# Optimization experiments

Measured on AMD Instinct MI355X. Metric: run time of the kernel, lower is better.

## Reference

```python
import jax, jax.numpy as jnp
import numpy as np

N = 50000      # nodes
E = 800000     # edges (before self-loops)
IN = 128       # in_channels
HID = 32       # hidden_channels
HEADS = 4
OUT = 2        # out_channels
NEG_SLOPE = 0.2  # PyG GATConv default LeakyReLU slope


def gat_layer(x, src, dst, W, a_src, a_dst, b, n_nodes, concat):
    """PyG GATConv (eval mode, self-loops already appended to src/dst).
    x: [N, in], W: [in, H*F], a_src/a_dst: [H, F], b: [H*F] or [F].
    """
    H, F = a_src.shape
    h = (x @ W).reshape(n_nodes, H, F)              # [N, H, F]
    al_s = (h * a_src).sum(-1)                      # [N, H] per-node src logit
    al_d = (h * a_dst).sum(-1)                      # [N, H] per-node dst logit
    e = al_s[src] + al_d[dst]                       # [E', H]
    e = jnp.where(e > 0, e, NEG_SLOPE * e)          # LeakyReLU
    # segment softmax over edges grouped by destination node
    m = jax.ops.segment_max(e, dst, num_segments=n_nodes)
    m = jnp.where(jnp.isfinite(m), m, 0.0)
    num = jnp.exp(e - m[dst])                       # [E', H]
    den = jax.ops.segment_sum(num, dst, num_segments=n_nodes)
    alpha = num / (den[dst] + 1e-16)                # [E', H]
    out = jax.ops.segment_sum(alpha[:, :, None] * h[src], dst, num_segments=n_nodes)  # [N, H, F]
    out = out.reshape(n_nodes, H * F) if concat else out.mean(axis=1)
    return out + b


def setup_inputs() -> dict:
    key = jax.random.key(0)
    ks = jax.random.split(key, 16)
    HID4 = HID // 4
    inp = {
        "x": jax.random.normal(ks[0], (N, IN), dtype=jnp.float32),
        "edge_index": jax.random.randint(ks[1], (2, E), 0, N, dtype=jnp.int64),
        "edge_attr": jax.random.normal(ks[2], (E, 8), dtype=jnp.float32),
        # conv1: in=IN -> HID per head, HEADS heads, concat
        "W1": jax.random.normal(ks[3], (IN, HEADS * HID), dtype=jnp.float32) * (1.0 / np.sqrt(IN)),
        "a_src1": jax.random.normal(ks[4], (HEADS, HID), dtype=jnp.float32) * 0.1,
        "a_dst1": jax.random.normal(ks[5], (HEADS, HID), dtype=jnp.float32) * 0.1,
        "b1": jnp.zeros((HEADS * HID,), dtype=jnp.float32),
        # conv2: in=HEADS*HID -> HID//4, 1 head, mean (concat=False)
        "W2": jax.random.normal(ks[6], (HEADS * HID, HID4), dtype=jnp.float32) * (1.0 / np.sqrt(HEADS * HID)),
        "a_src2": jax.random.normal(ks[7], (1, HID4), dtype=jnp.float32) * 0.1,
        "a_dst2": jax.random.normal(ks[8], (1, HID4), dtype=jnp.float32) * 0.1,
        "b2": jnp.zeros((HID4,), dtype=jnp.float32),
        # final linear
        "Wl": jax.random.normal(ks[9], (HID4, OUT), dtype=jnp.float32) * (1.0 / np.sqrt(HID4)),
        "bl": jnp.zeros((OUT,), dtype=jnp.float32),
    }
    return inp


def reference(x, edge_index, edge_attr, W1, a_src1, a_dst1, b1,
              W2, a_src2, a_dst2, b2, Wl, bl):
    # edge_attr is ignored (GATConv built without edge_dim). Eval mode: dropout is identity.
    loop = jnp.arange(N, dtype=edge_index.dtype)
    src = jnp.concatenate([edge_index[0], loop])  # PyG adds self-loops by default
    dst = jnp.concatenate([edge_index[1], loop])
    h = jax.nn.elu(gat_layer(x, src, dst, W1, a_src1, a_dst1, b1, N, concat=True))
    h = jax.nn.elu(gat_layer(h, src, dst, W2, a_src2, a_dst2, b2, N, concat=False))
    return jax.nn.sigmoid(h @ Wl + bl)
```

## Files before the change

### kernel.cpp

```cpp
#include <hip/hip_runtime.h>
#include <math.h>

#define TPB 256
#define BN 64
#define BK 32
#define CAP 64
#define LOG2E 1.44269504088896f

__device__ __forceinline__ float elu_f(float x)  { return x > 0.f ? x : __expf(x) - 1.f; }
__device__ __forceinline__ float sigmoid_f(float x){ return 1.f / (1.f + __expf(-x)); }
__device__ __forceinline__ float leaky(float x)  { return fmaxf(x, 0.2f * x); }

__device__ __forceinline__ unsigned int f2bf(float f) {
    unsigned int u = __float_as_uint(f);
    return (u + 0x7FFFu + ((u >> 16) & 1u)) >> 16;
}
__device__ __forceinline__ float bf_lo(unsigned int u) { return __uint_as_float(u << 16); }
__device__ __forceinline__ float bf_hi(unsigned int u) { return __uint_as_float(u & 0xffff0000u); }

static inline int cdiv(long long a, int b) { return (int)((a + b - 1) / b); }

__global__ __launch_bounds__(256) void gemm1_tiled(
        const float* __restrict__ x, const float* __restrict__ W,
        const float* __restrict__ a_src, const float* __restrict__ a_dst,
        unsigned short* __restrict__ hb, float* __restrict__ als, float* __restrict__ ald,
        int* __restrict__ cursor, int N) {
    if (threadIdx.x < BN) {
        int i = blockIdx.x * BN + threadIdx.x;
        if (i < N) cursor[i] = 0;
    }
    __shared__ float xs[BN][BK + 1];
    __shared__ float wsh[BK][128];
    int tid = threadIdx.x;
    int tx = tid & 15, ty = tid >> 4;
    int n0 = blockIdx.x * BN;

    float acc[4][8];
#pragma unroll
    for (int r = 0; r < 4; r++)
#pragma unroll
        for (int c = 0; c < 8; c++) acc[r][c] = 0.f;

    for (int k0 = 0; k0 < 128; k0 += BK) {
#pragma unroll
        for (int i = 0; i < 2; i++) {
            int r = (tid >> 3) + i * 32;
            int kk = (tid & 7) * 4;
            int row = n0 + r;
            float4 v = (row < N) ? *(const float4*)(x + (size_t)row * 128 + k0 + kk)
                                 : make_float4(0.f, 0.f, 0.f, 0.f);
            *(float4*)(&xs[r][kk]) = v;
        }
#pragma unroll
        for (int i = 0; i < 4; i++) {
            int idx = tid + i * 256;
            int kr = idx >> 5, c4 = (idx & 31) * 4;
            *(float4*)(&wsh[kr][c4]) = *(const float4*)(W + (size_t)(k0 + kr) * 128 + c4);
        }
        __syncthreads();
#pragma unroll
        for (int k = 0; k < BK; k++) {
            float a[4], bf[8];
#pragma unroll
            for (int i = 0; i < 4; i++) a[i] = xs[ty * 4 + i][k];
            float4 b0 = *(const float4*)(&wsh[k][tx * 8]);
            float4 b1 = *(const float4*)(&wsh[k][tx * 8 + 4]);
            bf[0] = b0.x; bf[1] = b0.y; bf[2] = b0.z; bf[3] = b0.w;
            bf[4] = b1.x; bf[5] = b1.y; bf[6] = b1.z; bf[7] = b1.w;
#pragma unroll
            for (int r = 0; r < 4; r++)
#pragma unroll
                for (int c = 0; c < 8; c++)
                    acc[r][c] = fmaf(a[r], bf[c], acc[r][c]);
        }
        __syncthreads();
    }

    float asr[8], adr[8];
#pragma unroll
    for (int i = 0; i < 8; i++) {
        asr[i] = a_src[tx * 8 + i];
        adr[i] = a_dst[tx * 8 + i];
    }
    int hd = tx >> 2;
#pragma unroll
    for (int r = 0; r < 4; r++) {
        int row = n0 + ty * 4 + r;
        float ps = 0.f, pd = 0.f;
#pragma unroll
        for (int i = 0; i < 8; i++) {
            ps = fmaf(acc[r][i], asr[i], ps);
            pd = fmaf(acc[r][i], adr[i], pd);
        }
        ps += __shfl_xor(ps, 1); ps += __shfl_xor(ps, 2);
        pd += __shfl_xor(pd, 1); pd += __shfl_xor(pd, 2);
        if (row < N) {
            uint4 o;
            o.x = f2bf(acc[r][0]) | (f2bf(acc[r][1]) << 16);
            o.y = f2bf(acc[r][2]) | (f2bf(acc[r][3]) << 16);
            o.z = f2bf(acc[r][4]) | (f2bf(acc[r][5]) << 16);
            o.w = f2bf(acc[r][6]) | (f2bf(acc[r][7]) << 16);
            *(uint4*)(hb + (size_t)row * 128 + tx * 8) = o;
            if ((tx & 3) == 0) {
                als[row * 4 + hd] = ps * LOG2E;
                ald[row * 4 + hd] = pd * LOG2E;
            }
        }
    }
}

__global__ void scatter_kernel(const int* __restrict__ ei, int E, int N, int gsz,
                               int* __restrict__ cursor, unsigned short* __restrict__ slots) {
    int myg = blockIdx.x & 7;
    int e = (blockIdx.x >> 3) * blockDim.x + threadIdx.x;
    if (e >= E + N) return;
    int d = (e < E) ? ei[E + e] : (e - E);
    if (d / gsz != myg) return;
    int s = (e < E) ? ei[e] : d;
    int pos = atomicAdd(&cursor[d], 1);
    if (pos < CAP) slots[((size_t)d << 6) + pos] = (unsigned short)s;
}

__global__ void accum1_fused(const int* __restrict__ cursor, const unsigned short* __restrict__ slots,
                             const unsigned short* __restrict__ hb,
                             const float* __restrict__ als, const float* __restrict__ ald,
                             const float* __restrict__ b, const float* __restrict__ W2,
                             const float* __restrict__ a_src2, const float* __restrict__ a_dst2,
                             float* __restrict__ h2, float* __restrict__ als2,
                             float* __restrict__ ald2, int N) {
    int t = blockIdx.x * blockDim.x + threadIdx.x;
    int n = t >> 6;
    if (n >= N) return;
    int lane = t & 63;
    int eslot = lane >> 4;
    int fg = lane & 15;
    int hd = fg >> 2;

    float ald_h = ald[n * 4 + hd];
    int cnt = cursor[n];
    const unsigned short* cp = slots + ((size_t)n << 6);

    int i0 = eslot < cnt ? eslot : cnt - 1;
    int s_c = cp[i0];
    float al_c = als[s_c * 4 + hd];
    uint4 u_c = *(const uint4*)(hb + (size_t)s_c * 128 + fg * 8);

    float acc[8];
#pragma unroll
    for (int k = 0; k < 8; k++) acc[k] = 0.f;
    float den = 0.f;

    for (int base = 0; base < cnt; base += 4) {
        int nxt = base + 4 + eslot;
        int ic = nxt < cnt ? nxt : cnt - 1;
        int s_n = cp[ic];
        float al_n = als[s_n * 4 + hd];
        uint4 u_n = *(const uint4*)(hb + (size_t)s_n * 128 + fg * 8);

        float w = exp2f(leaky(al_c + ald_h));
        if (base + eslot >= cnt) w = 0.f;
        acc[0] = fmaf(w, bf_lo(u_c.x), acc[0]);
        acc[1] = fmaf(w, bf_hi(u_c.x), acc[1]);
        acc[2] = fmaf(w, bf_lo(u_c.y), acc[2]);
        acc[3] = fmaf(w, bf_hi(u_c.y), acc[3]);
        acc[4] = fmaf(w, bf_lo(u_c.z), acc[4]);
        acc[5] = fmaf(w, bf_hi(u_c.z), acc[5]);
        acc[6] = fmaf(w, bf_lo(u_c.w), acc[6]);
        acc[7] = fmaf(w, bf_hi(u_c.w), acc[7]);
        den += w;

        al_c = al_n; u_c = u_n;
    }

#pragma unroll
    for (int k = 0; k < 8; k++) {
        acc[k] += __shfl_xor(acc[k], 16);
        acc[k] += __shfl_xor(acc[k], 32);
    }
    den += __shfl_xor(den, 16);
    den += __shfl_xor(den, 32);

    float inv = 1.f / (den + 1e-16f);
    float bv[8];
    *(float4*)(bv)     = *(const float4*)(b + fg * 8);
    *(float4*)(bv + 4) = *(const float4*)(b + fg * 8 + 4);
    float o[8];
#pragma unroll
    for (int k = 0; k < 8; k++) o[k] = elu_f(acc[k] * inv + bv[k]);

    int srcl = lane >> 2;
    float tmp[8];
#pragma unroll
    for (int k = 0; k < 8; k++) tmp[k] = __shfl(o[k], srcl);
    int sel = lane & 3;
    float o0 = sel == 0 ? tmp[0] : sel == 1 ? tmp[2] : sel == 2 ? tmp[4] : tmp[6];
    float o1 = sel == 0 ? tmp[1] : sel == 1 ? tmp[3] : sel == 2 ? tmp[5] : tmp[7];

    float w2a[8], w2b[8];
#pragma unroll
    for (int c = 0; c < 8; c += 4) {
        *(float4*)(w2a + c) = *(const float4*)(W2 + (size_t)(2 * lane) * 8 + c);
        *(float4*)(w2b + c) = *(const float4*)(W2 + (size_t)(2 * lane + 1) * 8 + c);
    }
    float part[8];
#pragma unroll
    for (int c = 0; c < 8; c++)
        part[c] = fmaf(o0, w2a[c], o1 * w2b[c]);
#pragma unroll
    for (int c = 0; c < 8; c++) {
        part[c] += __shfl_xor(part[c], 1);
        part[c] += __shfl_xor(part[c], 2);
        part[c] += __shfl_xor(part[c], 4);
    }
    int ch = lane & 7;
    float v = part[0];
    v = ch == 1 ? part[1] : v;  v = ch == 2 ? part[2] : v;  v = ch == 3 ? part[3] : v;
    v = ch == 4 ? part[4] : v;  v = ch == 5 ? part[5] : v;  v = ch == 6 ? part[6] : v;
    v = ch == 7 ? part[7] : v;
    v += __shfl_xor(v, 8); v += __shfl_xor(v, 16); v += __shfl_xor(v, 32);
    if (lane < 8) h2[(size_t)n * 8 + lane] = v;
    float ps = v * a_src2[ch];
    float pd = v * a_dst2[ch];
    ps += __shfl_xor(ps, 1); ps += __shfl_xor(ps, 2); ps += __shfl_xor(ps, 4);
    pd += __shfl_xor(pd, 1); pd += __shfl_xor(pd, 2); pd += __shfl_xor(pd, 4);
    if (lane == 0) {
        als2[n] = ps * LOG2E;
        ald2[n] = pd * LOG2E;
    }
}

__global__ void accum2_final(const int* __restrict__ cursor, const unsigned short* __restrict__ slots,
                             const float* __restrict__ h2,
                             const float* __restrict__ als, const float* __restrict__ ald,
                             const float* __restrict__ b2, const float* __restrict__ Wl,
                             const float* __restrict__ bl, float* __restrict__ out, int N) {
    int t = blockIdx.x * blockDim.x + threadIdx.x;
    int n = t >> 6;
    if (n >= N) return;
    int lane = t & 63;
    int slot = lane >> 3;
    int c = lane & 7;

    float ald_n = ald[n];
    int cnt = cursor[n];
    const unsigned short* cp = slots + ((size_t)n << 6);

    int i0 = slot < cnt ? slot : cnt - 1;
    int s_c = cp[i0];
    float al_c = als[s_c];
    float h_c = h2[(size_t)s_c * 8 + c];

    float den = 0.f, acc = 0.f;
    for (int base = 0; base < cnt; base += 8) {
        int nxt = base + 8 + slot;
        int ic = nxt < cnt ? nxt : cnt - 1;
        int s_n = cp[ic];
        float al_n = als[s_n];
        float h_n = h2[(size_t)s_n * 8 + c];

        float w = exp2f(leaky(al_c + ald_n));
        if (base + slot >= cnt) w = 0.f;
        acc = fmaf(w, h_c, acc);
        den += w;

        al_c = al_n; h_c = h_n;
    }
    acc += __shfl_xor(acc, 8);  acc += __shfl_xor(acc, 16); acc += __shfl_xor(acc, 32);
    den += __shfl_xor(den, 8);  den += __shfl_xor(den, 16); den += __shfl_xor(den, 32);

    float inv = 1.f / (den + 1e-16f);
    float o = elu_f(acc * inv + b2[c]);
    float r0 = o * Wl[c * 2 + 0];
    float r1 = o * Wl[c * 2 + 1];
    r0 += __shfl_xor(r0, 1); r0 += __shfl_xor(r0, 2); r0 += __shfl_xor(r0, 4);
    r1 += __shfl_xor(r1, 1); r1 += __shfl_xor(r1, 2); r1 += __shfl_xor(r1, 4);
    if (lane == 0) {
        float2 r;
        r.x = sigmoid_f(r0 + bl[0]);
        r.y = sigmoid_f(r1 + bl[1]);
        *(float2*)(out + (size_t)n * 2) = r;
    }
}

extern "C" void kernel_launch(void* const* d_in, const int* in_sizes, int n_in,
                              void* d_out, int out_size, void* d_ws, size_t ws_size,
                              hipStream_t stream) {
    const float* x      = (const float*)d_in[0];
    const int*   ei     = (const int*)d_in[1];
    const float* W1     = (const float*)d_in[3];
    const float* a_src1 = (const float*)d_in[4];
    const float* a_dst1 = (const float*)d_in[5];
    const float* b1     = (const float*)d_in[6];
    const float* W2     = (const float*)d_in[7];
    const float* a_src2 = (const float*)d_in[8];
    const float* a_dst2 = (const float*)d_in[9];
    const float* b2     = (const float*)d_in[10];
    const float* Wl     = (const float*)d_in[11];
    const float* bl     = (const float*)d_in[12];
    float* out = (float*)d_out;

    const int N = in_sizes[0] / 128;
    const int E = in_sizes[1] / 2;
    const int EN = E + N;
    const int gsz = cdiv(N, 8);

    unsigned short* h1b = (unsigned short*)d_ws;
    float* als1 = (float*)d_ws + (size_t)N * 64;
    float* ald1 = als1 + (size_t)N * 4;
    float* h2   = ald1 + (size_t)N * 4;
    float* als2 = h2   + (size_t)N * 8;
    float* ald2 = als2 + (size_t)N;
    int* cursor = (int*)(ald2 + (size_t)N);
    unsigned short* slots = (unsigned short*)(cursor + N);
    (void)ws_size; (void)n_in; (void)out_size;

    gemm1_tiled<<<cdiv(N, BN), 256, 0, stream>>>(x, W1, a_src1, a_dst1, h1b, als1, ald1, cursor, N);
    scatter_kernel<<<8 * cdiv(EN, TPB), TPB, 0, stream>>>(ei, E, N, gsz, cursor, slots);
    accum1_fused<<<cdiv((long long)N * 64, TPB), TPB, 0, stream>>>(
        cursor, slots, h1b, als1, ald1, b1, W2, a_src2, a_dst2, h2, als2, ald2, N);
    accum2_final<<<cdiv((long long)N * 64, TPB), TPB, 0, stream>>>(
        cursor, slots, h2, als2, ald2, b2, Wl, bl, out, N);
}
```

Baseline: 236.2 us.

## Use bf16 MFMA for first GEMM, handle self-loops inline, two edges per scatter thread

Replaces the FP32 tiled GEMM with a bf16 MFMA 16x16x32 kernel. x and a transposed W are staged as bf16 in shared memory, and the attention logits are reduced with shuffles. Self-loops are no longer scattered into slots; the accumulation kernels add the self-term directly, so each node's slot list and the atomic traffic shrink. The scatter kernel now handles two edges per thread and replaces the integer group divide with a float multiply. Rounding the GEMM inputs to bf16 lowers precision, and the float-based group test could misassign nodes at group boundaries.

After: 235.7 us. No clear change (-0.2%).

```diff
diff --git a/kernel.cpp b/kernel.cpp
--- a/kernel.cpp
+++ b/kernel.cpp
@@ -2,123 +2,148 @@
 #include <math.h>
 
 #define TPB 256
-#define BN 64
-#define BK 32
+#define GN 64
 #define CAP 64
 #define LOG2E 1.44269504088896f
+
+typedef short bf16x8 __attribute__((ext_vector_type(8)));
+typedef float floatx4 __attribute__((ext_vector_type(4)));
 
 __device__ __forceinline__ float elu_f(float x)  { return x > 0.f ? x : __expf(x) - 1.f; }
 __device__ __forceinline__ float sigmoid_f(float x){ return 1.f / (1.f + __expf(-x)); }
 __device__ __forceinline__ float leaky(float x)  { return fmaxf(x, 0.2f * x); }
 
-__device__ __forceinline__ unsigned int f2bf(float f) {
+__device__ __forceinline__ unsigned short f2bf(float f) {
     unsigned int u = __float_as_uint(f);
-    return (u + 0x7FFFu + ((u >> 16) & 1u)) >> 16;
+    return (unsigned short)((u + 0x7FFFu + ((u >> 16) & 1u)) >> 16);
 }
 __device__ __forceinline__ float bf_lo(unsigned int u) { return __uint_as_float(u << 16); }
 __device__ __forceinline__ float bf_hi(unsigned int u) { return __uint_as_float(u & 0xffff0000u); }
 
 static inline int cdiv(long long a, int b) { return (int)((a + b - 1) / b); }
 
-__global__ __launch_bounds__(256) void gemm1_tiled(
+__global__ __launch_bounds__(256) void gemm1_mfma(
         const float* __restrict__ x, const float* __restrict__ W,
         const float* __restrict__ a_src, const float* __restrict__ a_dst,
         unsigned short* __restrict__ hb, float* __restrict__ als, float* __restrict__ ald,
         int* __restrict__ cursor, int N) {
-    if (threadIdx.x < BN) {
-        int i = blockIdx.x * BN + threadIdx.x;
-        if (i < N) cursor[i] = 0;
-    }
-    __shared__ float xs[BN][BK + 1];
-    __shared__ float wsh[BK][128];
+    __shared__ unsigned short xs[GN][136];
+    __shared__ unsigned short wt[128][136];
     int tid = threadIdx.x;
-    int tx = tid & 15, ty = tid >> 4;
-    int n0 = blockIdx.x * BN;
-
-    float acc[4][8];
-#pragma unroll
-    for (int r = 0; r < 4; r++)
-#pragma unroll
-        for (int c = 0; c < 8; c++) acc[r][c] = 0.f;
-
-    for (int k0 = 0; k0 < 128; k0 += BK) {
-#pragma unroll
-        for (int i = 0; i < 2; i++) {
-            int r = (tid >> 3) + i * 32;
-            int kk = (tid & 7) * 4;
-            int row = n0 + r;
-            float4 v = (row < N) ? *(const float4*)(x + (size_t)row * 128 + k0 + kk)
-                                 : make_float4(0.f, 0.f, 0.f, 0.f);
-            *(float4*)(&xs[r][kk]) = v;
-        }
-#pragma unroll
-        for (int i = 0; i < 4; i++) {
-            int idx = tid + i * 256;
-            int kr = idx >> 5, c4 = (idx & 31) * 4;
-            *(float4*)(&wsh[kr][c4]) = *(const float4*)(W + (size_t)(k0 + kr) * 128 + c4);
-        }
-        __syncthreads();
-#pragma unroll
-        for (int k = 0; k < BK; k++) {
-            float a[4], bf[8];
-#pragma unroll
-            for (int i = 0; i < 4; i++) a[i] = xs[ty * 4 + i][k];
-            float4 b0 = *(const float4*)(&wsh[k][tx * 8]);
-            float4 b1 = *(const float4*)(&wsh[k][tx * 8 + 4]);
-            bf[0] = b0.x; bf[1] = b0.y; bf[2] = b0.z; bf[3] = b0.w;
-            bf[4] = b1.x; bf[5] = b1.y; bf[6] = b1.z; bf[7] = b1.w;
-#pragma unroll
-            for (int r = 0; r < 4; r++)
-#pragma unroll
-                for (int c = 0; c < 8; c++)
-                    acc[r][c] = fmaf(a[r], bf[c], acc[r][c]);
-        }
-        __syncthreads();
+    int n0 = blockIdx.x * GN;
+    if (tid < GN) { int i = n0 + tid; if (i < N) cursor[i] = 0; }
+
+#pragma unroll
+    for (int i = 0; i < 8; i++) {
+        int idx = tid + i * 256;
+        int r = idx >> 5;
+        int c4 = (idx & 31) * 4;
+        int row = n0 + r; if (row >= N) row = N - 1;
+        float4 v = *(const float4*)(x + (size_t)row * 128 + c4);
+        unsigned short* p = &xs[r][c4];
+        p[0] = f2bf(v.x); p[1] = f2bf(v.y); p[2] = f2bf(v.z); p[3] = f2bf(v.w);
+    }
+#pragma unroll
+    for (int i = 0; i < 16; i++) {
+        int idx = tid + i * 256;
+        int k = idx >> 5;
+        int c4 = (idx & 31) * 4;
+        float4 v = *(const float4*)(W + (size_t)k * 128 + c4);
+        wt[c4 + 0][k] = f2bf(v.x);
+        wt[c4 + 1][k] = f2bf(v.y);
+        wt[c4 + 2][k] = f2bf(v.z);
+        wt[c4 + 3][k] = f2bf(v.w);
+    }
+    __syncthreads();
+
+    int w = tid >> 6;
+    int lane = tid & 63;
+    int idx16 = lane & 15, quad = lane >> 4;
+    int nw = n0 + w * 16;
+
+    bf16x8 af[4];
+#pragma unroll
+    for (int kc = 0; kc < 4; kc++)
+        af[kc] = *(const bf16x8*)(&xs[w * 16 + idx16][kc * 32 + quad * 8]);
+
+    floatx4 accs[8];
+#pragma unroll
+    for (int cg = 0; cg < 8; cg++) {
+        floatx4 acc = {0.f, 0.f, 0.f, 0.f};
+#pragma unroll
+        for (int kc = 0; kc < 4; kc++) {
+            bf16x8 bf = *(const bf16x8*)(&wt[cg * 16 + idx16][kc * 32 + quad * 8]);
+            acc = __builtin_amdgcn_mfma_f32_16x16x32_bf16(af[kc], bf, acc, 0, 0, 0);
+        }
+        accs[cg] = acc;
     }
 
     float asr[8], adr[8];
 #pragma unroll
-    for (int i = 0; i < 8; i++) {
-        asr[i] = a_src[tx * 8 + i];
-        adr[i] = a_dst[tx * 8 + i];
-    }
-    int hd = tx >> 2;
-#pragma unroll
-    for (int r = 0; r < 4; r++) {
-        int row = n0 + ty * 4 + r;
-        float ps = 0.f, pd = 0.f;
-#pragma unroll
-        for (int i = 0; i < 8; i++) {
-            ps = fmaf(acc[r][i], asr[i], ps);
-            pd = fmaf(acc[r][i], adr[i], pd);
-        }
-        ps += __shfl_xor(ps, 1); ps += __shfl_xor(ps, 2);
-        pd += __shfl_xor(pd, 1); pd += __shfl_xor(pd, 2);
-        if (row < N) {
-            uint4 o;
-            o.x = f2bf(acc[r][0]) | (f2bf(acc[r][1]) << 16);
-            o.y = f2bf(acc[r][2]) | (f2bf(acc[r][3]) << 16);
-            o.z = f2bf(acc[r][4]) | (f2bf(acc[r][5]) << 16);
-            o.w = f2bf(acc[r][6]) | (f2bf(acc[r][7]) << 16);
-            *(uint4*)(hb + (size_t)row * 128 + tx * 8) = o;
-            if ((tx & 3) == 0) {
-                als[row * 4 + hd] = ps * LOG2E;
-                ald[row * 4 + hd] = pd * LOG2E;
-            }
-        }
-    }
-}
-
-__global__ void scatter_kernel(const int* __restrict__ ei, int E, int N, int gsz,
+    for (int cg = 0; cg < 8; cg++) {
+        asr[cg] = a_src[cg * 16 + idx16];
+        adr[cg] = a_dst[cg * 16 + idx16];
+    }
+    float ps[16], pd[16];
+#pragma unroll
+    for (int i = 0; i < 16; i++) { ps[i] = 0.f; pd[i] = 0.f; }
+#pragma unroll
+    for (int cg = 0; cg < 8; cg++) {
+        int h = cg >> 1;
+#pragma unroll
+        for (int r = 0; r < 4; r++) {
+            ps[r * 4 + h] = fmaf(accs[cg][r], asr[cg], ps[r * 4 + h]);
+            pd[r * 4 + h] = fmaf(accs[cg][r], adr[cg], pd[r * 4 + h]);
+        }
+    }
+#pragma unroll
+    for (int i = 0; i < 16; i++) {
+        ps[i] += __shfl_xor(ps[i], 1); ps[i] += __shfl_xor(ps[i], 2);
+        ps[i] += __shfl_xor(ps[i], 4); ps[i] += __shfl_xor(ps[i], 8);
+        pd[i] += __shfl_xor(pd[i], 1); pd[i] += __shfl_xor(pd[i], 2);
+        pd[i] += __shfl_xor(pd[i], 4); pd[i] += __shfl_xor(pd[i], 8);
+    }
+    float myps = 0.f, mypd = 0.f;
+#pragma unroll
+    for (int i = 0; i < 16; i++) {
+        if (i == idx16) { myps = ps[i]; mypd = pd[i]; }
+    }
+    int rowl = nw + quad * 4 + (idx16 >> 2);
+    if (rowl < N) {
+        als[rowl * 4 + (idx16 & 3)] = myps * LOG2E;
+        ald[rowl * 4 + (idx16 & 3)] = mypd * LOG2E;
+    }
+#pragma unroll
+    for (int cg = 0; cg < 8; cg++) {
+#pragma unroll
+        for (int r = 0; r < 4; r++) {
+            int row = nw + quad * 4 + r;
+            if (row < N) hb[(size_t)row * 128 + cg * 16 + idx16] = f2bf(accs[cg][r]);
+        }
+    }
+}
+
+__global__ void scatter_kernel(const int* __restrict__ ei, int E, float invg,
                                int* __restrict__ cursor, unsigned short* __restrict__ slots) {
     int myg = blockIdx.x & 7;
-    int e = (blockIdx.x >> 3) * blockDim.x + threadIdx.x;
-    if (e >= E + N) return;
-    int d = (e < E) ? ei[E + e] : (e - E);
-    if (d / gsz != myg) return;
-    int s = (e < E) ? ei[e] : d;
-    int pos = atomicAdd(&cursor[d], 1);
-    if (pos < CAP) slots[((size_t)d << 6) + pos] = (unsigned short)s;
+    int p = (blockIdx.x >> 3) * blockDim.x + threadIdx.x;
+    int e0 = p * 2;
+    if (e0 >= E) return;
+    int d0 = ei[E + e0];
+    if ((int)((float)d0 * invg) == myg) {
+        int s = ei[e0];
+        int pos = atomicAdd(&cursor[d0], 1);
+        if (pos < CAP) slots[((size_t)d0 << 6) + pos] = (unsigned short)s;
+    }
+    int e1 = e0 + 1;
+    if (e1 < E) {
+        int d1 = ei[E + e1];
+        if ((int)((float)d1 * invg) == myg) {
+            int s = ei[e1];
+            int pos = atomicAdd(&cursor[d1], 1);
+            if (pos < CAP) slots[((size_t)d1 << 6) + pos] = (unsigned short)s;
+        }
+    }
 }
 
 __global__ void accum1_fused(const int* __restrict__ cursor, const unsigned short* __restrict__ slots,
@@ -140,36 +165,46 @@
     int cnt = cursor[n];
     const unsigned short* cp = slots + ((size_t)n << 6);
 
-    int i0 = eslot < cnt ? eslot : cnt - 1;
-    int s_c = cp[i0];
-    float al_c = als[s_c * 4 + hd];
-    uint4 u_c = *(const uint4*)(hb + (size_t)s_c * 128 + fg * 8);
-
     float acc[8];
 #pragma unroll
     for (int k = 0; k < 8; k++) acc[k] = 0.f;
     float den = 0.f;
-
-    for (int base = 0; base < cnt; base += 4) {
-        int nxt = base + 4 + eslot;
-        int ic = nxt < cnt ? nxt : cnt - 1;
-        int s_n = cp[ic];
-        float al_n = als[s_n * 4 + hd];
-        uint4 u_n = *(const uint4*)(hb + (size_t)s_n * 128 + fg * 8);
-
-        float w = exp2f(leaky(al_c + ald_h));
-        if (base + eslot >= cnt) w = 0.f;
-        acc[0] = fmaf(w, bf_lo(u_c.x), acc[0]);
-        acc[1] = fmaf(w, bf_hi(u_c.x), acc[1]);
-        acc[2] = fmaf(w, bf_lo(u_c.y), acc[2]);
-        acc[3] = fmaf(w, bf_hi(u_c.y), acc[3]);
-        acc[4] = fmaf(w, bf_lo(u_c.z), acc[4]);
-        acc[5] = fmaf(w, bf_hi(u_c.z), acc[5]);
-        acc[6] = fmaf(w, bf_lo(u_c.w), acc[6]);
-        acc[7] = fmaf(w, bf_hi(u_c.w), acc[7]);
-        den += w;
-
-        al_c = al_n; u_c = u_n;
+    if (eslot == 0) {
+        float wself = exp2f(leaky(als[n * 4 + hd] + ald_h));
+        uint4 us = *(const uint4*)(hb + (size_t)n * 128 + fg * 8);
+        acc[0] = wself * bf_lo(us.x); acc[1] = wself * bf_hi(us.x);
+        acc[2] = wself * bf_lo(us.y); acc[3] = wself * bf_hi(us.y);
+        acc[4] = wself * bf_lo(us.z); acc[5] = wself * bf_hi(us.z);
+        acc[6] = wself * bf_lo(us.w); acc[7] = wself * bf_hi(us.w);
+        den = wself;
+    }
+
+    if (cnt > 0) {
+        int i0 = eslot < cnt ? eslot : cnt - 1;
+        int s_c = cp[i0];
+        float al_c = als[s_c * 4 + hd];
+        uint4 u_c = *(const uint4*)(hb + (size_t)s_c * 128 + fg * 8);
+        for (int base = 0; base < cnt; base += 4) {
+            int nxt = base + 4 + eslot;
+            int ic = nxt < cnt ? nxt : cnt - 1;
+            int s_n = cp[ic];
+            float al_n = als[s_n * 4 + hd];
+            uint4 u_n = *(const uint4*)(hb + (size_t)s_n * 128 + fg * 8);
+
+            float w = exp2f(leaky(al_c + ald_h));
+            if (base + eslot >= cnt) w = 0.f;
+            acc[0] = fmaf(w, bf_lo(u_c.x), acc[0]);
+            acc[1] = fmaf(w, bf_hi(u_c.x), acc[1]);
+            acc[2] = fmaf(w, bf_lo(u_c.y), acc[2]);
+            acc[3] = fmaf(w, bf_hi(u_c.y), acc[3]);
+            acc[4] = fmaf(w, bf_lo(u_c.z), acc[4]);
+            acc[5] = fmaf(w, bf_hi(u_c.z), acc[5]);
+            acc[6] = fmaf(w, bf_lo(u_c.w), acc[6]);
+            acc[7] = fmaf(w, bf_hi(u_c.w), acc[7]);
+            den += w;
+
+            al_c = al_n; u_c = u_n;
+        }
     }
 
 #pragma unroll
@@ -245,25 +280,32 @@
     int cnt = cursor[n];
     const unsigned short* cp = slots + ((size_t)n << 6);
 
-    int i0 = slot < cnt ? slot : cnt - 1;
-    int s_c = cp[i0];
-    float al_c = als[s_c];
-    float h_c = h2[(size_t)s_c * 8 + c];
-
     float den = 0.f, acc = 0.f;
-    for (int base = 0; base < cnt; base += 8) {
-        int nxt = base + 8 + slot;
-        int ic = nxt < cnt ? nxt : cnt - 1;
-        int s_n = cp[ic];
-        float al_n = als[s_n];
-        float h_n = h2[(size_t)s_n * 8 + c];
-
-        float w = exp2f(leaky(al_c + ald_n));
-        if (base + slot >= cnt) w = 0.f;
-        acc = fmaf(w, h_c, acc);
-        den += w;
-
-        al_c = al_n; h_c = h_n;
+    if (slot == 0) {
+        float wself = exp2f(leaky(als[n] + ald_n));
+        acc = wself * h2[(size_t)n * 8 + c];
+        den = wself;
+    }
+
+    if (cnt > 0) {
+        int i0 = slot < cnt ? slot : cnt - 1;
+        int s_c = cp[i0];
+        float al_c = als[s_c];
+        float h_c = h2[(size_t)s_c * 8 + c];
+        for (int base = 0; base < cnt; base += 8) {
+            int nxt = base + 8 + slot;
+            int ic = nxt < cnt ? nxt : cnt - 1;
+            int s_n = cp[ic];
+            float al_n = als[s_n];
+            float h_n = h2[(size_t)s_n * 8 + c];
+
+            float w = exp2f(leaky(al_c + ald_n));
+            if (base + slot >= cnt) w = 0.f;
+            acc = fmaf(w, h_c, acc);
+            den += w;
+
+            al_c = al_n; h_c = h_n;
+        }
     }
     acc += __shfl_xor(acc, 8);  acc += __shfl_xor(acc, 16); acc += __shfl_xor(acc, 32);
     den += __shfl_xor(den, 8);  den += __shfl_xor(den, 16); den += __shfl_xor(den, 32);
@@ -301,8 +343,8 @@
 
     const int N = in_sizes[0] / 128;
     const int E = in_sizes[1] / 2;
-    const int EN = E + N;
     const int gsz = cdiv(N, 8);
+    const float invg = 1.f / (float)gsz;
 
     unsigned short* h1b = (unsigned short*)d_ws;
     float* als1 = (float*)d_ws + (size_t)N * 64;
@@ -314,8 +356,8 @@
     unsigned short* slots = (unsigned short*)(cursor + N);
     (void)ws_size; (void)n_in; (void)out_size;
 
-    gemm1_tiled<<<cdiv(N, BN), 256, 0, stream>>>(x, W1, a_src1, a_dst1, h1b, als1, ald1, cursor, N);
-    scatter_kernel<<<8 * cdiv(EN, TPB), TPB, 0, stream>>>(ei, E, N, gsz, cursor, slots);
+    gemm1_mfma<<<cdiv(N, GN), 256, 0, stream>>>(x, W1, a_src1, a_dst1, h1b, als1, ald1, cursor, N);
+    scatter_kernel<<<8 * cdiv(cdiv(E, 2), TPB), TPB, 0, stream>>>(ei, E, invg, cursor, slots);
     accum1_fused<<<cdiv((long long)N * 64, TPB), TPB, 0, stream>>>(
         cursor, slots, h1b, als1, ald1, b1, W2, a_src2, a_dst2, h2, als2, ald2, N);
     accum2_final<<<cdiv((long long)N * 64, TPB), TPB, 0, stream>>>(
```
